# Kernel optimization log

Hardware: AMD Instinct MI355X
Metric: run time of the kernel (lower is better)

## Reference

```python
import jax, jax.numpy as jnp
import numpy as np

N_NODES = 100000
N_EDGES = 3200000
IN_F = 256
OUT_F = 256


def setup_inputs() -> dict:
    key = jax.random.key(0)
    k1, k2, k3, k4, k5 = jax.random.split(key, 5)
    input_ = jax.random.normal(k1, (N_NODES, IN_F), dtype=jnp.float32)
    edge_src = jax.random.randint(k2, (N_EDGES,), 0, N_NODES, dtype=jnp.int64)
    edge_dst = jax.random.randint(k3, (N_EDGES,), 0, N_NODES, dtype=jnp.int64)
    edge_val = jax.random.uniform(k4, (N_EDGES,), dtype=jnp.float32)
    stdv = 1.0 / np.sqrt(OUT_F)
    weight = jax.random.uniform(k5, (IN_F, OUT_F), dtype=jnp.float32,
                                minval=-stdv, maxval=stdv)
    return {"input_": input_, "edge_src": edge_src, "edge_dst": edge_dst,
            "edge_val": edge_val, "weight": weight}


def reference(input_, edge_src, edge_dst, edge_val, weight):
    # neighbor = spmm(adj, input_): adj in COO form (dst, src, val)
    gathered = edge_val[:, None] * input_[edge_src]          # [E, F]
    neighbor = jax.ops.segment_sum(gathered, edge_dst,
                                   num_segments=N_NODES)     # [N, F]
    ft_input = input_ @ weight                               # [N, O]
    ft_neighbor = neighbor @ weight                          # [N, O]
    return jnp.concatenate([ft_input, ft_neighbor], axis=1)  # [N, 2*O]
```

## Files before the change

### kernel.cpp

```cpp
#include <hip/hip_runtime.h>
#include <hip/hip_fp16.h>

#define N_NODES 100000
#define N_EDGES 3200000
#define F 256

#define BM 64
#define BN 256
#define BK 32

#define MAX_DEG 80
#define INIT_NB ((N_NODES + 255) / 256)
#define EDGE_NB4 (N_EDGES / 1024)
#define GEMM_NB ((N_NODES + BM - 1) / BM)
#define FUSED_NB (GEMM_NB + EDGE_NB4)

typedef __attribute__((ext_vector_type(8))) short short8;
typedef __attribute__((ext_vector_type(4))) float f32x4;

__device__ inline unsigned short f2bf(float f) {
    unsigned int u = __float_as_uint(f);
    unsigned int r = (u + 0x7fffu + ((u >> 16) & 1u)) >> 16;
    return (unsigned short)r;
}

__device__ inline float bf2f(unsigned short b) {
    return __uint_as_float(((unsigned int)b) << 16);
}

__device__ inline unsigned int pack_rec(int src, float val) {
    __half h = __float2half(val);
    unsigned short hb = *reinterpret_cast<unsigned short*>(&h);
    return ((unsigned int)src << 15) | (unsigned int)hb;
}

__device__ inline int rec_src(unsigned int p) { return (int)(p >> 15); }

__device__ inline float rec_val(unsigned int p) {
    unsigned short hb = (unsigned short)(p & 0x7FFFu);
    __half h = *reinterpret_cast<__half*>(&hb);
    return __half2float(h);
}

__global__ __launch_bounds__(256)
void init_kernel(const float* __restrict__ W, unsigned short* __restrict__ Wt,
                 int* __restrict__ counts) {
    const int idx = blockIdx.x * 256 + threadIdx.x;
    if (idx < N_NODES) counts[idx] = 0;
    if (idx < 256 * 256) {
        const int n = idx >> 8;
        const int k = idx & 255;
        Wt[n * 256 + k] = f2bf(W[k * 256 + n]);
    }
}

__global__ __launch_bounds__(256, 3)
void gemm_bucket_kernel(const float* __restrict__ A,
                        const unsigned short* __restrict__ Wt,
                        float* __restrict__ out,
                        unsigned short* __restrict__ ftb,
                        const int* __restrict__ src,
                        const int* __restrict__ dst,
                        const float* __restrict__ val,
                        int* __restrict__ counts,
                        unsigned int* __restrict__ recs)
{
    __shared__ unsigned short As[BM * BK];
    __shared__ unsigned short Bs[BN * BK];

    const int bid = blockIdx.x;

    if (bid % 3 != 0) {
        const int ebid = 2 * (bid / 3) + (bid % 3) - 1;
        const int e0 = (ebid * 256 + threadIdx.x) * 4;
        const int4   s = *(const int4*)(src + e0);
        const int4   d = *(const int4*)(dst + e0);
        const float4 v = *(const float4*)(val + e0);
        const int r0 = atomicAdd(&counts[d.x], 1);
        const int r1 = atomicAdd(&counts[d.y], 1);
        const int r2 = atomicAdd(&counts[d.z], 1);
        const int r3 = atomicAdd(&counts[d.w], 1);
        if (r0 < MAX_DEG) recs[d.x * MAX_DEG + r0] = pack_rec(s.x, v.x);
        if (r1 < MAX_DEG) recs[d.y * MAX_DEG + r1] = pack_rec(s.y, v.y);
        if (r2 < MAX_DEG) recs[d.z * MAX_DEG + r2] = pack_rec(s.z, v.z);
        if (r3 < MAX_DEG) recs[d.w * MAX_DEG + r3] = pack_rec(s.w, v.w);
        return;
    }

    const int tid   = threadIdx.x;
    const int lane  = tid & 63;
    const int wave  = tid >> 6;
    const int waveM = wave >> 1;
    const int waveN = wave & 1;
    const int rowBase = (bid / 3) * BM;

    f32x4 acc[2][8];
#pragma unroll
    for (int i = 0; i < 2; i++)
#pragma unroll
        for (int j = 0; j < 8; j++) acc[i][j] = (f32x4)0.0f;

    const int sr = tid >> 2;
    const int sk = (tid & 3) * 8;
    const int quad = lane >> 4;
    const int l16  = lane & 15;

    for (int kt = 0; kt < 8; kt++) {
        const int k0 = kt * BK;
        {
            const int grow = rowBase + sr;
            short8 av;
            if (grow < N_NODES) {
                const float4* pa = (const float4*)(A + (size_t)grow * 256 + k0 + sk);
                float4 f0 = pa[0];
                float4 f1 = pa[1];
                av[0] = (short)f2bf(f0.x); av[1] = (short)f2bf(f0.y);
                av[2] = (short)f2bf(f0.z); av[3] = (short)f2bf(f0.w);
                av[4] = (short)f2bf(f1.x); av[5] = (short)f2bf(f1.y);
                av[6] = (short)f2bf(f1.z); av[7] = (short)f2bf(f1.w);
            } else {
                av = (short8)0;
            }
            *(short8*)(&As[sr * BK + sk]) = av;
        }
#pragma unroll
        for (int p = 0; p < 4; p++) {
            const int r = p * 64 + sr;
            const uint4 wv = *(const uint4*)(Wt + (size_t)r * 256 + k0 + sk);
            *(uint4*)(&Bs[r * BK + sk]) = wv;
        }
        __syncthreads();

        short8 af[2], bfr[8];
#pragma unroll
        for (int i = 0; i < 2; i++)
            af[i] = *(const short8*)(&As[(waveM * 32 + i * 16 + l16) * BK + quad * 8]);
#pragma unroll
        for (int j = 0; j < 8; j++)
            bfr[j] = *(const short8*)(&Bs[(waveN * 128 + j * 16 + l16) * BK + quad * 8]);
#pragma unroll
        for (int i = 0; i < 2; i++)
#pragma unroll
            for (int j = 0; j < 8; j++)
                acc[i][j] = __builtin_amdgcn_mfma_f32_16x16x32_bf16(
                    bfr[j], af[i], acc[i][j], 0, 0, 0);
        __syncthreads();
    }

#pragma unroll
    for (int i = 0; i < 2; i++) {
        const int row = rowBase + waveM * 32 + i * 16 + l16;
        if (row < N_NODES) {
#pragma unroll
            for (int j = 0; j < 8; j++) {
                const int col = waveN * 128 + j * 16 + quad * 4;
                f32x4 v = acc[i][j];
                *(f32x4*)(out + (size_t)row * 512 + col) = v;
                unsigned int p0 = ((unsigned int)f2bf(v[1]) << 16) | f2bf(v[0]);
                unsigned int p1 = ((unsigned int)f2bf(v[3]) << 16) | f2bf(v[2]);
                *(uint2*)(ftb + (size_t)row * 256 + col) = make_uint2(p0, p1);
            }
        }
    }
}

__global__ __launch_bounds__(256)
void gather_kernel(const int* __restrict__ counts,
                   const unsigned int* __restrict__ recs,
                   const unsigned short* __restrict__ ftb,
                   float* __restrict__ out)
{
    const int n = blockIdx.x * 4 + (threadIdx.x >> 6);
    if (n >= N_NODES) return;
    const int lane = threadIdx.x & 63;

    int len = counts[n];
    if (len > MAX_DEG) len = MAX_DEG;
    const unsigned int* rp = recs + (size_t)n * MAX_DEG;

    float ax = 0.f, ay = 0.f, az = 0.f, aw = 0.f;

    int e = 0;

    if (e + 7 < len) {
        unsigned int r[8];
#pragma unroll
        for (int q = 0; q < 8; q++) r[q] = rp[e + q];
        while (true) {
            const int en = e + 8;
            const bool moreN = (en + 7 < len);
            unsigned int rn[8];
            if (moreN) {
#pragma unroll
                for (int q = 0; q < 8; q++) rn[q] = rp[en + q];
            }
            ushort4 u[8];
#pragma unroll
            for (int q = 0; q < 8; q++)
                u[q] = *(const ushort4*)(ftb + (size_t)rec_src(r[q]) * 256 + lane * 4);
#pragma unroll
            for (int q = 0; q < 8; q++) {
                const float v = rec_val(r[q]);
                ax += v * bf2f(u[q].x); ay += v * bf2f(u[q].y);
                az += v * bf2f(u[q].z); aw += v * bf2f(u[q].w);
            }
            e = en;
            if (!moreN) break;
#pragma unroll
            for (int q = 0; q < 8; q++) r[q] = rn[q];
        }
    }

    for (; e + 3 < len; e += 4) {
        unsigned int r0 = rp[e];
        unsigned int r1 = rp[e + 1];
        unsigned int r2 = rp[e + 2];
        unsigned int r3 = rp[e + 3];
        ushort4 u0 = *(const ushort4*)(ftb + (size_t)rec_src(r0) * 256 + lane * 4);
        ushort4 u1 = *(const ushort4*)(ftb + (size_t)rec_src(r1) * 256 + lane * 4);
        ushort4 u2 = *(const ushort4*)(ftb + (size_t)rec_src(r2) * 256 + lane * 4);
        ushort4 u3 = *(const ushort4*)(ftb + (size_t)rec_src(r3) * 256 + lane * 4);
        const float v0 = rec_val(r0);
        const float v1 = rec_val(r1);
        const float v2 = rec_val(r2);
        const float v3 = rec_val(r3);
        ax += v0 * bf2f(u0.x); ay += v0 * bf2f(u0.y);
        az += v0 * bf2f(u0.z); aw += v0 * bf2f(u0.w);
        ax += v1 * bf2f(u1.x); ay += v1 * bf2f(u1.y);
        az += v1 * bf2f(u1.z); aw += v1 * bf2f(u1.w);
        ax += v2 * bf2f(u2.x); ay += v2 * bf2f(u2.y);
        az += v2 * bf2f(u2.z); aw += v2 * bf2f(u2.w);
        ax += v3 * bf2f(u3.x); ay += v3 * bf2f(u3.y);
        az += v3 * bf2f(u3.z); aw += v3 * bf2f(u3.w);
    }
    for (; e < len; e++) {
        unsigned int r0 = rp[e];
        ushort4 u0 = *(const ushort4*)(ftb + (size_t)rec_src(r0) * 256 + lane * 4);
        const float v0 = rec_val(r0);
        ax += v0 * bf2f(u0.x); ay += v0 * bf2f(u0.y);
        az += v0 * bf2f(u0.z); aw += v0 * bf2f(u0.w);
    }

    float4 res = make_float4(ax, ay, az, aw);
    *(float4*)(out + (size_t)n * 512 + 256 + lane * 4) = res;
}

extern "C" void kernel_launch(void* const* d_in, const int* in_sizes, int n_in,
                              void* d_out, int out_size, void* d_ws, size_t ws_size,
                              hipStream_t stream)
{
    const float* input = (const float*)d_in[0];
    const int*   esrc  = (const int*)d_in[1];
    const int*   edst  = (const int*)d_in[2];
    const float* eval  = (const float*)d_in[3];
    const float* W     = (const float*)d_in[4];
    float* out = (float*)d_out;

    char* ws = (char*)d_ws;
    unsigned short* Wt  = (unsigned short*)(ws);
    int* counts         = (int*)(ws + 131072);
    unsigned int* recs  = (unsigned int*)(ws + 532480);
    unsigned short* ftb = (unsigned short*)(ws + 32532480);

    init_kernel<<<INIT_NB, 256, 0, stream>>>(W, Wt, counts);

    gemm_bucket_kernel<<<FUSED_NB, 256, 0, stream>>>(
        input, Wt, out, ftb, esrc, edst, eval, counts, recs);

    gather_kernel<<<(N_NODES + 3) / 4, 256, 0, stream>>>(counts, recs, ftb, out);
}
```

Measured before the change: 618.4 us.

## Load GEMM MFMA fragments directly from global memory, drop LDS staging

The GEMM path no longer stages A and W tiles in shared memory with barriers. Each wave now loads its MFMA operand fragments straight from global memory into registers. This removes LDS traffic, the LDS footprint and both __syncthreads per k-step, which can raise occupancy and let these blocks coexist better with the edge-bucketing blocks. In exchange, A rows are read by both waveN waves and the W fragments are re-read by every wave from global memory or cache, with less coalesced 16-byte strided accesses.

```diff
diff --git a/kernel.cpp b/kernel.cpp
--- a/kernel.cpp
+++ b/kernel.cpp
@@ -65,9 +65,6 @@
                         int* __restrict__ counts,
                         unsigned int* __restrict__ recs)
 {
-    __shared__ unsigned short As[BM * BK];
-    __shared__ unsigned short Bs[BN * BK];
-
     const int bid = blockIdx.x;
 
     if (bid % 3 != 0) {
@@ -94,26 +91,35 @@
     const int waveN = wave & 1;
     const int rowBase = (bid / 3) * BM;
 
-    f32x4 acc[2][8];
-#pragma unroll
-    for (int i = 0; i < 2; i++)
-#pragma unroll
-        for (int j = 0; j < 8; j++) acc[i][j] = (f32x4)0.0f;
-
-    const int sr = tid >> 2;
-    const int sk = (tid & 3) * 8;
     const int quad = lane >> 4;
     const int l16  = lane & 15;
 
+    f32x4 acc[2][8];
+#pragma unroll
+    for (int i = 0; i < 2; i++)
+#pragma unroll
+        for (int j = 0; j < 8; j++) acc[i][j] = (f32x4)0.0f;
+
+    const int row0 = rowBase + waveM * 32 + l16;
+    const int row1 = row0 + 16;
+    const bool ok0 = row0 < N_NODES;
+    const bool ok1 = row1 < N_NODES;
+    const float* pa0 = A + (size_t)row0 * 256 + quad * 8;
+    const float* pa1 = A + (size_t)row1 * 256 + quad * 8;
+    const unsigned short* pb = Wt + (size_t)(waveN * 128 + l16) * 256 + quad * 8;
+
     for (int kt = 0; kt < 8; kt++) {
         const int k0 = kt * BK;
-        {
-            const int grow = rowBase + sr;
+
+        short8 af[2];
+#pragma unroll
+        for (int i = 0; i < 2; i++) {
+            const float* pa = (i == 0) ? pa0 : pa1;
+            const bool ok = (i == 0) ? ok0 : ok1;
             short8 av;
-            if (grow < N_NODES) {
-                const float4* pa = (const float4*)(A + (size_t)grow * 256 + k0 + sk);
-                float4 f0 = pa[0];
-                float4 f1 = pa[1];
+            if (ok) {
+                const float4 f0 = *(const float4*)(pa + k0);
+                const float4 f1 = *(const float4*)(pa + k0 + 4);
                 av[0] = (short)f2bf(f0.x); av[1] = (short)f2bf(f0.y);
                 av[2] = (short)f2bf(f0.z); av[3] = (short)f2bf(f0.w);
                 av[4] = (short)f2bf(f1.x); av[5] = (short)f2bf(f1.y);
@@ -121,30 +127,20 @@
             } else {
                 av = (short8)0;
             }
-            *(short8*)(&As[sr * BK + sk]) = av;
+            af[i] = av;
         }
-#pragma unroll
-        for (int p = 0; p < 4; p++) {
-            const int r = p * 64 + sr;
-            const uint4 wv = *(const uint4*)(Wt + (size_t)r * 256 + k0 + sk);
-            *(uint4*)(&Bs[r * BK + sk]) = wv;
-        }
-        __syncthreads();
-
-        short8 af[2], bfr[8];
-#pragma unroll
-        for (int i = 0; i < 2; i++)
-            af[i] = *(const short8*)(&As[(waveM * 32 + i * 16 + l16) * BK + quad * 8]);
+
+        short8 bfr[8];
 #pragma unroll
         for (int j = 0; j < 8; j++)
-            bfr[j] = *(const short8*)(&Bs[(waveN * 128 + j * 16 + l16) * BK + quad * 8]);
+            bfr[j] = *(const short8*)(pb + (size_t)(j * 16) * 256 + k0);
+
 #pragma unroll
         for (int i = 0; i < 2; i++)
 #pragma unroll
             for (int j = 0; j < 8; j++)
                 acc[i][j] = __builtin_amdgcn_mfma_f32_16x16x32_bf16(
                     bfr[j], af[i], acc[i][j], 0, 0, 0);
-        __syncthreads();
     }
 
 #pragma unroll
```

Result: slower. 710.2 us (+14.8%).
